# Kernel tuning notes

Measured on AMD Instinct MI355X. Metric: run time of the kernel, lower is better.

The kernel has to match this reference:

```python
import jax, jax.numpy as jnp
import numpy as np

N_CHEM = 50000
N_GENE = 50000
D = 256   # input embed size per ntype
H = 256   # hidden size
O = 256   # out size
E = 400000  # edges per etype
ETYPES = [("chemical", "ch2ge", "gene"),
          ("gene", "ge2ch", "chemical"),
          ("chemical", "ch2ch", "chemical"),
          ("gene", "ge2ge", "gene")]
N_NODES = {"chemical": N_CHEM, "gene": N_GENE}


def setup_inputs() -> dict:
    key = jax.random.key(0)
    ks = jax.random.split(key, 40)
    inp = {}
    inp["chemical_embed"] = jax.random.normal(ks[0], (N_CHEM, D), jnp.float32)
    inp["gene_embed"] = jax.random.normal(ks[1], (N_GENE, D), jnp.float32)
    i = 2
    for st, et, dt in ETYPES:
        inp[f"W1_{et}"] = jax.random.normal(ks[i], (D, H), jnp.float32) / np.float32(np.sqrt(D)); i += 1
        inp[f"b1_{et}"] = jnp.zeros((H,), jnp.float32)
        inp[f"W2_{et}"] = jax.random.normal(ks[i], (H, O), jnp.float32) / np.float32(np.sqrt(H)); i += 1
        inp[f"b2_{et}"] = jnp.zeros((O,), jnp.float32)
        inp[f"src_{et}"] = jax.random.randint(ks[i], (E,), 0, N_NODES[st], jnp.int32); i += 1
        inp[f"dst_{et}"] = jax.random.randint(ks[i], (E,), 0, N_NODES[dt], jnp.int32); i += 1
    return inp


def _rgcn_layer(h, Ws, bs, srcs, dsts):
    """One HeteroRGCNLayer: per-etype linear on src feats, copy_u + mean reduce,
    then sum across etypes per destination ntype (DGL multi_update_all 'sum')."""
    out_dim = Ws[0].shape[1]
    dt_ref = h[ETYPES[0][0]].dtype
    agg = {nt: jnp.zeros((n, out_dim), dt_ref) for nt, n in N_NODES.items()}
    for (st, et, dt), W, b, s_idx, d_idx in zip(ETYPES, Ws, bs, srcs, dsts):
        Wh = h[st] @ W + b                              # [N_src, out]
        msg = Wh[s_idx]                                 # [E, out] gather
        ssum = jax.ops.segment_sum(msg, d_idx, num_segments=N_NODES[dt])
        cnt = jax.ops.segment_sum(jnp.ones((s_idx.shape[0], 1), dt_ref), d_idx,
                                  num_segments=N_NODES[dt])
        agg[dt] = agg[dt] + ssum / jnp.maximum(cnt, 1.0)  # mean per etype
    return agg


def reference(chemical_embed, gene_embed,
              W1_ch2ge, b1_ch2ge, W1_ge2ch, b1_ge2ch, W1_ch2ch, b1_ch2ch, W1_ge2ge, b1_ge2ge,
              W2_ch2ge, b2_ch2ge, W2_ge2ch, b2_ge2ch, W2_ch2ch, b2_ch2ch, W2_ge2ge, b2_ge2ge,
              src_ch2ge, dst_ch2ge, src_ge2ch, dst_ge2ch, src_ch2ch, dst_ch2ch, src_ge2ge, dst_ge2ge):
    srcs = [src_ch2ge, src_ge2ch, src_ch2ch, src_ge2ge]
    dsts = [dst_ch2ge, dst_ge2ch, dst_ch2ch, dst_ge2ge]
    W1s = [W1_ch2ge, W1_ge2ch, W1_ch2ch, W1_ge2ge]
    b1s = [b1_ch2ge, b1_ge2ch, b1_ch2ch, b1_ge2ge]
    W2s = [W2_ch2ge, W2_ge2ch, W2_ch2ch, W2_ge2ge]
    b2s = [b2_ch2ge, b2_ge2ch, b2_ch2ch, b2_ge2ge]

    h = {"chemical": chemical_embed, "gene": gene_embed}
    h = _rgcn_layer(h, W1s, b1s, srcs, dsts)
    h = {k: jax.nn.leaky_relu(v, negative_slope=0.01) for k, v in h.items()}
    h = _rgcn_layer(h, W2s, b2s, srcs, dsts)
    return h["chemical"]
```

## Files before the change

kernel.cpp:

```cpp
#include <hip/hip_runtime.h>
#include <hip/hip_bf16.h>

#define NNODE 50000
#define DIM   256
#define EDGES 400000
#define NET   4
#define NTOT  (NET * NNODE)
#define BSH   7
#define NBUCK ((NTOT + 127) >> BSH)
#define EPB2  8192
#define CPE   49
#define NBLKT (CPE * NET)
#define NSCAN (NBUCK * NBLKT)

#define AS1 __attribute__((address_space(1)))
#define AS3 __attribute__((address_space(3)))

typedef __attribute__((ext_vector_type(8))) __bf16 bf16x8;
typedef __attribute__((ext_vector_type(4))) float f32x4;
typedef __attribute__((ext_vector_type(4))) unsigned short u16x4;
typedef __attribute__((ext_vector_type(8))) unsigned short u16x8;

__device__ __forceinline__ float bf2f(unsigned short u) {
  unsigned int x = ((unsigned int)u) << 16;
  return __builtin_bit_cast(float, x);
}
__device__ __forceinline__ unsigned short f2bf(float f) {
  __hip_bfloat16 h = __float2bfloat16(f);
  return __builtin_bit_cast(unsigned short, h);
}

__global__ void conv_f32_bf16(const float* __restrict__ in, unsigned short* __restrict__ out, int n4) {
  int i = blockIdx.x * blockDim.x + threadIdx.x;
  if (i >= n4) return;
  f32x4 v = reinterpret_cast<const f32x4*>(in)[i];
  u16x4 o;
  o[0] = f2bf(v[0]); o[1] = f2bf(v[1]); o[2] = f2bf(v[2]); o[3] = f2bf(v[3]);
  reinterpret_cast<u16x4*>(out)[i] = o;
}

__global__ void conv_wTb(const float* __restrict__ a0, const float* __restrict__ b0,
                         const float* __restrict__ a1, const float* __restrict__ b1,
                         const float* __restrict__ a2, const float* __restrict__ b2,
                         unsigned short* __restrict__ t0, unsigned short* __restrict__ t1,
                         unsigned short* __restrict__ t2) {
  int m = blockIdx.y;
  const float* A = (m == 0) ? a0 : (m == 1) ? a1 : a2;
  const float* B = (m == 0) ? b0 : (m == 1) ? b1 : b2;
  unsigned short* T = (m == 0) ? t0 : (m == 1) ? t1 : t2;
  int n = blockIdx.x, k = threadIdx.x;
  int seg = ((k >> 3) & 7) ^ (n & 7), j = k & 7;
  T[((k >> 6) * 256 + n) * 64 + seg * 8 + j]       = f2bf(A[k * 256 + n]);
  T[((4 + (k >> 6)) * 256 + n) * 64 + seg * 8 + j] = f2bf(B[k * 256 + n]);
}

__global__ void fill_f32(float* __restrict__ p, float v, int n) {
  int i = blockIdx.x * blockDim.x + threadIdx.x;
  if (i < n) p[i] = v;
}

__global__ void hist_ms(const int* __restrict__ d0, const int* __restrict__ d1,
                        const int* __restrict__ d2, const int* __restrict__ d3,
                        int* __restrict__ cnt) {
  __shared__ int h[NBUCK];
  for (int i = threadIdx.x; i < NBUCK; i += 256) h[i] = 0;
  __syncthreads();
  int t = blockIdx.y, cx = blockIdx.x;
  const int* dp = (t == 0) ? d0 : (t == 1) ? d1 : (t == 2) ? d2 : d3;
  int base = cx * EPB2;
  int lim = base + EPB2; if (lim > EDGES) lim = EDGES;
  for (int i = base + threadIdx.x; i < lim; i += 256)
    atomicAdd(&h[(t * NNODE + dp[i]) >> BSH], 1);
  __syncthreads();
  int blk = t * CPE + cx;
  for (int i = threadIdx.x; i < NBUCK; i += 256)
    cnt[i * NBLKT + blk] = h[i];
}

__global__ void scan_p1(const int* __restrict__ data, int* __restrict__ bsum, int n) {
  __shared__ int red[256];
  int base = blockIdx.x * 4096;
  int s = 0;
  #pragma unroll
  for (int j = 0; j < 16; j++) {
    int idx = base + j * 256 + threadIdx.x;
    s += (idx < n) ? data[idx] : 0;
  }
  red[threadIdx.x] = s;
  __syncthreads();
  for (int o = 128; o > 0; o >>= 1) {
    if (threadIdx.x < o) red[threadIdx.x] += red[threadIdx.x + o];
    __syncthreads();
  }
  if (threadIdx.x == 0) bsum[blockIdx.x] = red[0];
}

__global__ void scan_p2(int* __restrict__ bsum, int nb, int* __restrict__ off, int nscan,
                        int* __restrict__ S) {
  __shared__ int sh[128];
  int tid = threadIdx.x;
  int v = (tid < nb) ? bsum[tid] : 0;
  sh[tid] = v;
  __syncthreads();
  for (int o = 1; o < 128; o <<= 1) {
    int a = (tid >= o) ? sh[tid - o] : 0;
    __syncthreads();
    sh[tid] += a;
    __syncthreads();
  }
  if (tid < nb) bsum[tid] = sh[tid] - v;
  if (tid == 0) { off[nscan] = sh[127]; S[NTOT] = sh[127]; }
}

__global__ void scan_p3(int* __restrict__ data, const int* __restrict__ bsum, int n) {
  __shared__ int sh[256];
  int tid = threadIdx.x;
  int base = blockIdx.x * 4096 + tid * 16;
  int vals[16];
  int s = 0;
  #pragma unroll
  for (int j = 0; j < 16; j++) {
    vals[j] = (base + j < n) ? data[base + j] : 0;
    s += vals[j];
  }
  sh[tid] = s;
  __syncthreads();
  for (int o = 1; o < 256; o <<= 1) {
    int a = (tid >= o) ? sh[tid - o] : 0;
    __syncthreads();
    sh[tid] += a;
    __syncthreads();
  }
  int run = bsum[blockIdx.x] + sh[tid] - s;
  #pragma unroll
  for (int j = 0; j < 16; j++) {
    if (base + j < n) { data[base + j] = run; run += vals[j]; }
  }
}

__global__ void scatter_ms(const int* __restrict__ s0, const int* __restrict__ s1,
                           const int* __restrict__ s2, const int* __restrict__ s3,
                           const int* __restrict__ d0, const int* __restrict__ d1,
                           const int* __restrict__ d2, const int* __restrict__ d3,
                           const int* __restrict__ off, unsigned int* __restrict__ pairs) {
  __shared__ int cur[NBUCK];
  int t = blockIdx.y, cx = blockIdx.x;
  int blk = t * CPE + cx;
  for (int i = threadIdx.x; i < NBUCK; i += 256)
    cur[i] = off[i * NBLKT + blk];
  __syncthreads();
  const int* sp = (t == 0) ? s0 : (t == 1) ? s1 : (t == 2) ? s2 : s3;
  const int* dp = (t == 0) ? d0 : (t == 1) ? d1 : (t == 2) ? d2 : d3;
  int base = cx * EPB2;
  int lim = base + EPB2; if (lim > EDGES) lim = EDGES;
  for (int i = base + threadIdx.x; i < lim; i += 256) {
    int key = t * NNODE + dp[i];
    int slot = atomicAdd(&cur[key >> BSH], 1);
    pairs[slot] = ((unsigned int)(key & 127) << 16) | (unsigned int)sp[i];
  }
}

__global__ void bucket_final(const int* __restrict__ off, const unsigned int* __restrict__ pairs,
                             int* __restrict__ S, int* __restrict__ srcs) {
  __shared__ int lcnt[128];
  __shared__ int loff[128];
  int b = blockIdx.x;
  int tid = threadIdx.x;
  int beg = off[b * NBLKT], end = off[(b + 1) * NBLKT];
  if (tid < 128) lcnt[tid] = 0;
  __syncthreads();
  for (int e = beg + tid; e < end; e += 256)
    atomicAdd(&lcnt[pairs[e] >> 16], 1);
  __syncthreads();
  int c = (tid < 128) ? lcnt[tid] : 0;
  if (tid < 128) loff[tid] = c;
  __syncthreads();
  for (int o = 1; o < 128; o <<= 1) {
    int a = (tid < 128 && tid >= o) ? loff[tid - o] : 0;
    __syncthreads();
    if (tid < 128) loff[tid] += a;
    __syncthreads();
  }
  if (tid < 128) {
    int ex = loff[tid] - c;
    int key = (b << BSH) + tid;
    if (key < NTOT) S[key] = beg + ex;
    lcnt[tid] = ex;
  }
  __syncthreads();
  for (int e = beg + tid; e < end; e += 256) {
    unsigned int p = pairs[e];
    int lk = p >> 16;
    int slot = beg + atomicAdd(&lcnt[lk], 1);
    srcs[slot] = (int)(p & 0xFFFFu);
  }
}

#define ACC8(V)                                             \
  { _Pragma("unroll")                                       \
    for (int j = 0; j < 8; j++) acc[j] += bf2f((V)[j]); }

__device__ __forceinline__ void agg_loop(const int* __restrict__ srcs, int e0, int e1,
                                         int half, int l5,
                                         const unsigned short* __restrict__ feat, float* acc) {
  int e = e0 + half;
  u16x8 z = {};
  #define LDK(K) ((e + 2*(K) < e1)                                                    \
      ? *reinterpret_cast<const u16x8*>(feat + (size_t)srcs[e + 2*(K)] * 256 + l5 * 8) \
      : z)
  u16x8 v0 = LDK(0), v1 = LDK(1), v2 = LDK(2), v3 = LDK(3);
  while (e + 8 < e1) {
    u16x8 c0 = v0, c1 = v1, c2 = v2, c3 = v3;
    e += 8;
    v0 = LDK(0); v1 = LDK(1); v2 = LDK(2); v3 = LDK(3);
    ACC8(c0); ACC8(c1); ACC8(c2); ACC8(c3);
  }
  ACC8(v0); ACC8(v1); ACC8(v2); ACC8(v3);
  #undef LDK
}

__global__ __launch_bounds__(256) void agg_pair(
    const int* __restrict__ S, const int* __restrict__ srcs,
    const unsigned short* __restrict__ featA, int etA, unsigned short* __restrict__ outA,
    const unsigned short* __restrict__ featB, int etB, unsigned short* __restrict__ outB)
{
  int d = blockIdx.x * 4 + (threadIdx.x >> 6);
  int lane = threadIdx.x & 63;
  int half = lane >> 5, l5 = lane & 31;
  size_t obase = ((size_t)(l5 >> 3) * NNODE + d) * 64 + (((l5 & 7) ^ (d & 7)) << 3);

  int gA = etA * NNODE + d;
  int a0 = S[gA], a1 = S[gA + 1];
  int gB = etB * NNODE + d;
  int b0 = S[gB], b1 = S[gB + 1];

  {
    float acc[8] = {0,0,0,0,0,0,0,0};
    agg_loop(srcs, a0, a1, half, l5, featA, acc);
    #pragma unroll
    for (int j = 0; j < 8; j++) acc[j] += __shfl_xor(acc[j], 32);
    float dA = (float)(a1 - a0); if (dA < 1.f) dA = 1.f;
    float invA = 1.f / dA;
    if (half == 0) {
      u16x8 o;
      #pragma unroll
      for (int j = 0; j < 8; j++) o[j] = f2bf(acc[j] * invA);
      *reinterpret_cast<u16x8*>(outA + obase) = o;
    }
  }
  {
    float acc[8] = {0,0,0,0,0,0,0,0};
    agg_loop(srcs, b0, b1, half, l5, featB, acc);
    #pragma unroll
    for (int j = 0; j < 8; j++) acc[j] += __shfl_xor(acc[j], 32);
    float dB = (float)(b1 - b0); if (dB < 1.f) dB = 1.f;
    float invB = 1.f / dB;
    if (half == 1) {
      u16x8 o;
      #pragma unroll
      for (int j = 0; j < 8; j++) o[j] = f2bf(acc[j] * invB);
      *reinterpret_cast<u16x8*>(outB + obase) = o;
    }
  }
}

template<int MODE>
__global__ __launch_bounds__(256, 2) void gemm512(
    const unsigned short* __restrict__ A0, const unsigned short* __restrict__ A1,
    const unsigned short* __restrict__ WTb,
    const float* __restrict__ bA, const float* __restrict__ bB,
    const int* __restrict__ S, int etA, int etB,
    void* __restrict__ outp, int M)
{
  __shared__ char lds[2 * 40960];
  int tid = threadIdx.x;
  int m0 = blockIdx.x * 64;
  int wave = tid >> 6, lane = tid & 63;
  int wr = wave >> 1, wc = wave & 1;
  int lrow = lane & 15, kgrp = lane >> 4;

  f32x4 acc[2][8];
  #pragma unroll
  for (int a = 0; a < 2; a++)
    #pragma unroll
    for (int b = 0; b < 8; b++) acc[a][b] = (f32x4){0.f, 0.f, 0.f, 0.f};

  auto stage = [&](int ck) {
    char* buf = lds + (ck & 1) * 40960;
    const char* wsrc = (const char*)WTb + (size_t)ck * 32768 + tid * 16;
    #pragma unroll
    for (int iss = 0; iss < 8; iss++)
      __builtin_amdgcn_global_load_lds(
          (const AS1 unsigned int*)(const void*)(wsrc + iss * 4096),
          (AS3 unsigned int*)(void*)(buf + 8192 + iss * 4096 + tid * 16), 16, 0, 0);
    const char* asrc = (const char*)((ck < 4) ? A0 : A1) +
        (size_t)(ck & 3) * NNODE * 128 + (size_t)m0 * 128 + tid * 16;
    #pragma unroll
    for (int iss = 0; iss < 2; iss++)
      __builtin_amdgcn_global_load_lds(
          (const AS1 unsigned int*)(const void*)(asrc + iss * 4096),
          (AS3 unsigned int*)(void*)(buf + iss * 4096 + tid * 16), 16, 0, 0);
  };

  auto compute = [&](int ck) {
    const char* buf = lds + (ck & 1) * 40960;
    #pragma unroll
    for (int ks = 0; ks < 2; ks++) {
      int ks4 = ks << 2;
      bf16x8 a[2];
      #pragma unroll
      for (int mb = 0; mb < 2; mb++) {
        int r = 32 * wr + 16 * mb + lrow;
        a[mb] = *reinterpret_cast<const bf16x8*>(buf + r * 128 + (((ks4 | kgrp) ^ (r & 7)) << 4));
      }
      #pragma unroll
      for (int nb = 0; nb < 8; nb++) {
        int n = 128 * wc + 16 * nb + lrow;
        bf16x8 b = *reinterpret_cast<const bf16x8*>(buf + 8192 + n * 128 + (((ks4 | kgrp) ^ (n & 7)) << 4));
        acc[0][nb] = __builtin_amdgcn_mfma_f32_16x16x32_bf16(a[0], b, acc[0][nb], 0, 0, 0);
        acc[1][nb] = __builtin_amdgcn_mfma_f32_16x16x32_bf16(a[1], b, acc[1][nb], 0, 0, 0);
      }
    }
  };

  stage(0);
  for (int ck = 0; ck < 7; ck++) {
    stage(ck + 1);
    asm volatile("s_waitcnt vmcnt(10)" ::: "memory");
    asm volatile("s_barrier" ::: "memory");
    compute(ck);
    asm volatile("s_barrier" ::: "memory");
  }
  asm volatile("s_waitcnt vmcnt(0)" ::: "memory");
  asm volatile("s_barrier" ::: "memory");
  compute(7);

  #pragma unroll
  for (int mb = 0; mb < 2; mb++) {
    #pragma unroll
    for (int r = 0; r < 4; r++) {
      int row = m0 + 32 * wr + 16 * mb + kgrp * 4 + r;
      if (row >= M) continue;
      int gA = etA * NNODE + row, gB = etB * NNODE + row;
      bool hA = S[gA + 1] > S[gA];
      bool hB = S[gB + 1] > S[gB];
      #pragma unroll
      for (int nb = 0; nb < 8; nb++) {
        int col = 128 * wc + 16 * nb + lrow;
        float bias = (hA ? bA[col] : 0.f) + (hB ? bB[col] : 0.f);
        float v = acc[mb][nb][r] + bias;
        if (MODE == 0) {
          v = (v > 0.f) ? v : 0.01f * v;
          ((unsigned short*)outp)[(size_t)row * 256 + col] = f2bf(v);
        } else {
          ((float*)outp)[(size_t)row * 256 + col] = v;
        }
      }
    }
  }
}

extern "C" void kernel_launch(void* const* d_in, const int* in_sizes, int n_in,
                              void* d_out, int out_size, void* d_ws, size_t ws_size,
                              hipStream_t stream) {
  (void)in_sizes; (void)n_in;
  const float* chem = (const float*)d_in[0];
  const float* gene = (const float*)d_in[1];
  const float *W1[4], *B1[4], *W2[4], *B2[4];
  const int *SRC[4], *DST[4];
  for (int t = 0; t < 4; t++) {
    W1[t]  = (const float*)d_in[2 + 6 * t];
    B1[t]  = (const float*)d_in[3 + 6 * t];
    W2[t]  = (const float*)d_in[4 + 6 * t];
    B2[t]  = (const float*)d_in[5 + 6 * t];
    SRC[t] = (const int*)d_in[6 + 6 * t];
    DST[t] = (const int*)d_in[7 + 6 * t];
  }

  size_t off_b = 0;
  auto carve = [&](size_t bytes) -> void* {
    void* p = (char*)d_ws + off_b;
    off_b += (bytes + 255) & ~(size_t)255;
    return p;
  };
  const size_t FEAT_B = (size_t)NNODE * DIM * 2;
  unsigned short* xb_chem = (unsigned short*)carve(FEAT_B);
  unsigned short* xb_gene = (unsigned short*)carve(FEAT_B);
  unsigned short* h1_chem = (unsigned short*)carve(FEAT_B);
  unsigned short* h1_gene = (unsigned short*)carve(FEAT_B);
  unsigned short* aggA    = (unsigned short*)carve(FEAT_B);
  unsigned short* aggB    = (unsigned short*)carve(FEAT_B);
  int* S    = (int*)carve(((size_t)NTOT + 1) * 4);
  int* srcs = (int*)carve((size_t)NET * EDGES * 4);
  unsigned short* WTc1 = (unsigned short*)carve((size_t)256 * 512 * 2);
  unsigned short* WTg1 = (unsigned short*)carve((size_t)256 * 512 * 2);
  unsigned short* WTc2 = (unsigned short*)carve((size_t)256 * 512 * 2);
  unsigned int* pairs = (unsigned int*)aggA;
  int* cntoff = (int*)((char*)aggA + 6400000);
  int* bsum   = cntoff + (NSCAN + 1);

  if (off_b > ws_size) {
    fill_f32<<<(out_size + 255) / 256, 256, 0, stream>>>((float*)d_out, (float)(ws_size >> 20), out_size);
    return;
  }

  int n4 = NNODE * DIM / 4;
  conv_f32_bf16<<<(n4 + 255) / 256, 256, 0, stream>>>(chem, xb_chem, n4);
  conv_f32_bf16<<<(n4 + 255) / 256, 256, 0, stream>>>(gene, xb_gene, n4);
  conv_wTb<<<dim3(256, 3), 256, 0, stream>>>(W1[1], W1[2], W1[0], W1[3], W2[1], W2[2],
                                             WTc1, WTg1, WTc2);

  dim3 cgrid(CPE, 4);
  hist_ms<<<cgrid, 256, 0, stream>>>(DST[0], DST[1], DST[2], DST[3], cntoff);
  int nb1 = (NSCAN + 4095) / 4096;
  scan_p1<<<nb1, 256, 0, stream>>>(cntoff, bsum, NSCAN);
  scan_p2<<<1, 128, 0, stream>>>(bsum, nb1, cntoff, NSCAN, S);
  scan_p3<<<nb1, 256, 0, stream>>>(cntoff, bsum, NSCAN);
  scatter_ms<<<cgrid, 256, 0, stream>>>(SRC[0], SRC[1], SRC[2], SRC[3],
                                        DST[0], DST[1], DST[2], DST[3], cntoff, pairs);
  bucket_final<<<NBUCK, 256, 0, stream>>>(cntoff, pairs, S, srcs);

  dim3 ggrid2((NNODE + 63) / 64);
  int nagg = NNODE / 4;
  agg_pair<<<nagg, 256, 0, stream>>>(S, srcs, xb_gene, 1, aggA, xb_chem, 2, aggB);
  gemm512<0><<<ggrid2, 256, 0, stream>>>(aggA, aggB, WTc1, B1[1], B1[2], S, 1, 2, h1_chem, NNODE);
  agg_pair<<<nagg, 256, 0, stream>>>(S, srcs, xb_chem, 0, aggA, xb_gene, 3, aggB);
  gemm512<0><<<ggrid2, 256, 0, stream>>>(aggA, aggB, WTg1, B1[0], B1[3], S, 0, 3, h1_gene, NNODE);
  agg_pair<<<nagg, 256, 0, stream>>>(S, srcs, h1_gene, 1, aggA, h1_chem, 2, aggB);
  gemm512<1><<<ggrid2, 256, 0, stream>>>(aggA, aggB, WTc2, B2[1], B2[2], S, 1, 2, d_out, NNODE);
}
```

Before: 427.3 us.

## Fuse neighbor mean-aggregation into GEMM via LDS-resident aggregated tile

Replaces the separate agg_pair and gemm512 kernels with a fused kernel. Each block of 32 destination rows aggregates its neighbor features into LDS and then runs the MFMA GEMM against double-buffered weight chunks streamed in 32-wide K slices. This removes the global write and re-read of the intermediate aggregated features and three kernel launches. In exchange the M tile shrinks from 64 to 32, so the weights are re-fetched by twice as many blocks, and the weight layout is re-swizzled for the narrower K chunks. The sort scratch moves into the h1_chem buffer.

```diff
diff --git a/kernel.cpp b/kernel.cpp
--- a/kernel.cpp
+++ b/kernel.cpp
@@ -39,19 +39,20 @@
   reinterpret_cast<u16x4*>(out)[i] = o;
 }
 
-__global__ void conv_wTb(const float* __restrict__ a0, const float* __restrict__ b0,
-                         const float* __restrict__ a1, const float* __restrict__ b1,
-                         const float* __restrict__ a2, const float* __restrict__ b2,
-                         unsigned short* __restrict__ t0, unsigned short* __restrict__ t1,
-                         unsigned short* __restrict__ t2) {
+__global__ void conv_wT32(const float* __restrict__ a0, const float* __restrict__ b0,
+                          const float* __restrict__ a1, const float* __restrict__ b1,
+                          const float* __restrict__ a2, const float* __restrict__ b2,
+                          unsigned short* __restrict__ t0, unsigned short* __restrict__ t1,
+                          unsigned short* __restrict__ t2) {
   int m = blockIdx.y;
   const float* A = (m == 0) ? a0 : (m == 1) ? a1 : a2;
   const float* B = (m == 0) ? b0 : (m == 1) ? b1 : b2;
   unsigned short* T = (m == 0) ? t0 : (m == 1) ? t1 : t2;
   int n = blockIdx.x, k = threadIdx.x;
-  int seg = ((k >> 3) & 7) ^ (n & 7), j = k & 7;
-  T[((k >> 6) * 256 + n) * 64 + seg * 8 + j]       = f2bf(A[k * 256 + n]);
-  T[((4 + (k >> 6)) * 256 + n) * 64 + seg * 8 + j] = f2bf(B[k * 256 + n]);
+  int kg = (k >> 3) & 3, j = k & 7;
+  int sw = ((kg ^ (n & 3)) << 3) + j;
+  T[(k >> 5) * 8192 + n * 32 + sw]       = f2bf(A[k * 256 + n]);
+  T[(8 + (k >> 5)) * 8192 + n * 32 + sw] = f2bf(B[k * 256 + n]);
 }
 
 __global__ void fill_f32(float* __restrict__ p, float v, int n) {
@@ -219,134 +220,110 @@
   #undef LDK
 }
 
-__global__ __launch_bounds__(256) void agg_pair(
+template<int MODE>
+__global__ __launch_bounds__(256, 2) void fused_ag(
     const int* __restrict__ S, const int* __restrict__ srcs,
-    const unsigned short* __restrict__ featA, int etA, unsigned short* __restrict__ outA,
-    const unsigned short* __restrict__ featB, int etB, unsigned short* __restrict__ outB)
-{
-  int d = blockIdx.x * 4 + (threadIdx.x >> 6);
-  int lane = threadIdx.x & 63;
-  int half = lane >> 5, l5 = lane & 31;
-  size_t obase = ((size_t)(l5 >> 3) * NNODE + d) * 64 + (((l5 & 7) ^ (d & 7)) << 3);
-
-  int gA = etA * NNODE + d;
-  int a0 = S[gA], a1 = S[gA + 1];
-  int gB = etB * NNODE + d;
-  int b0 = S[gB], b1 = S[gB + 1];
-
-  {
-    float acc[8] = {0,0,0,0,0,0,0,0};
-    agg_loop(srcs, a0, a1, half, l5, featA, acc);
-    #pragma unroll
-    for (int j = 0; j < 8; j++) acc[j] += __shfl_xor(acc[j], 32);
-    float dA = (float)(a1 - a0); if (dA < 1.f) dA = 1.f;
-    float invA = 1.f / dA;
-    if (half == 0) {
-      u16x8 o;
-      #pragma unroll
-      for (int j = 0; j < 8; j++) o[j] = f2bf(acc[j] * invA);
-      *reinterpret_cast<u16x8*>(outA + obase) = o;
-    }
-  }
-  {
-    float acc[8] = {0,0,0,0,0,0,0,0};
-    agg_loop(srcs, b0, b1, half, l5, featB, acc);
-    #pragma unroll
-    for (int j = 0; j < 8; j++) acc[j] += __shfl_xor(acc[j], 32);
-    float dB = (float)(b1 - b0); if (dB < 1.f) dB = 1.f;
-    float invB = 1.f / dB;
-    if (half == 1) {
-      u16x8 o;
-      #pragma unroll
-      for (int j = 0; j < 8; j++) o[j] = f2bf(acc[j] * invB);
-      *reinterpret_cast<u16x8*>(outB + obase) = o;
-    }
-  }
-}
-
-template<int MODE>
-__global__ __launch_bounds__(256, 2) void gemm512(
-    const unsigned short* __restrict__ A0, const unsigned short* __restrict__ A1,
+    const unsigned short* __restrict__ featA, int etA,
+    const unsigned short* __restrict__ featB, int etB,
     const unsigned short* __restrict__ WTb,
     const float* __restrict__ bA, const float* __restrict__ bB,
-    const int* __restrict__ S, int etA, int etB,
     void* __restrict__ outp, int M)
 {
-  __shared__ char lds[2 * 40960];
+  __shared__ char lds[32768 + 2 * 16384];
   int tid = threadIdx.x;
-  int m0 = blockIdx.x * 64;
   int wave = tid >> 6, lane = tid & 63;
-  int wr = wave >> 1, wc = wave & 1;
+  int half = lane >> 5, l5 = lane & 31;
   int lrow = lane & 15, kgrp = lane >> 4;
-
-  f32x4 acc[2][8];
+  int m0 = blockIdx.x * 32;
+
+  auto stageB = [&](int ck) {
+    char* buf = lds + 32768 + (ck & 1) * 16384;
+    const char* src = (const char*)WTb + (size_t)ck * 16384 + tid * 16;
+    #pragma unroll
+    for (int iss = 0; iss < 4; iss++)
+      __builtin_amdgcn_global_load_lds(
+          (const AS1 unsigned int*)(const void*)(src + iss * 4096),
+          (AS3 unsigned int*)(void*)(buf + iss * 4096 + tid * 16), 16, 0, 0);
+  };
+  stageB(0);
+
+  for (int i = 0; i < 8; i++) {
+    int r = wave * 8 + i;
+    int d = m0 + r;
+    int a0 = 0, a1 = 0, b0 = 0, b1 = 0;
+    if (d < M) {
+      int gA = etA * NNODE + d;
+      a0 = S[gA]; a1 = S[gA + 1];
+      int gB = etB * NNODE + d;
+      b0 = S[gB]; b1 = S[gB + 1];
+    }
+    float accA[8] = {0,0,0,0,0,0,0,0}, accB[8] = {0,0,0,0,0,0,0,0};
+    { float* acc = accA; agg_loop(srcs, a0, a1, half, l5, featA, acc); }
+    { float* acc = accB; agg_loop(srcs, b0, b1, half, l5, featB, acc); }
+    #pragma unroll
+    for (int j = 0; j < 8; j++) {
+      accA[j] += __shfl_xor(accA[j], 32);
+      accB[j] += __shfl_xor(accB[j], 32);
+    }
+    float dA = (float)(a1 - a0); if (dA < 1.f) dA = 1.f;
+    float dB = (float)(b1 - b0); if (dB < 1.f) dB = 1.f;
+    float invA = 1.f / dA, invB = 1.f / dB;
+    u16x8 o;
+    int s;
+    if (half == 0) {
+      #pragma unroll
+      for (int j = 0; j < 8; j++) o[j] = f2bf(accA[j] * invA);
+      s = l5;
+    } else {
+      #pragma unroll
+      for (int j = 0; j < 8; j++) o[j] = f2bf(accB[j] * invB);
+      s = 32 + l5;
+    }
+    *reinterpret_cast<u16x8*>(lds + r * 1024 + ((s ^ (r & 7)) << 4)) = o;
+  }
+
+  f32x4 acc[2][4];
   #pragma unroll
   for (int a = 0; a < 2; a++)
     #pragma unroll
-    for (int b = 0; b < 8; b++) acc[a][b] = (f32x4){0.f, 0.f, 0.f, 0.f};
-
-  auto stage = [&](int ck) {
-    char* buf = lds + (ck & 1) * 40960;
-    const char* wsrc = (const char*)WTb + (size_t)ck * 32768 + tid * 16;
-    #pragma unroll
-    for (int iss = 0; iss < 8; iss++)
-      __builtin_amdgcn_global_load_lds(
-          (const AS1 unsigned int*)(const void*)(wsrc + iss * 4096),
-          (AS3 unsigned int*)(void*)(buf + 8192 + iss * 4096 + tid * 16), 16, 0, 0);
-    const char* asrc = (const char*)((ck < 4) ? A0 : A1) +
-        (size_t)(ck & 3) * NNODE * 128 + (size_t)m0 * 128 + tid * 16;
-    #pragma unroll
-    for (int iss = 0; iss < 2; iss++)
-      __builtin_amdgcn_global_load_lds(
-          (const AS1 unsigned int*)(const void*)(asrc + iss * 4096),
-          (AS3 unsigned int*)(void*)(buf + iss * 4096 + tid * 16), 16, 0, 0);
+    for (int b = 0; b < 4; b++) acc[a][b] = (f32x4){0.f, 0.f, 0.f, 0.f};
+
+  auto compute = [&](int ck) {
+    const char* bbuf = lds + 32768 + (ck & 1) * 16384;
+    int kseg = ck * 4 + kgrp;
+    bf16x8 a[2];
+    #pragma unroll
+    for (int mb = 0; mb < 2; mb++) {
+      int r = mb * 16 + lrow;
+      a[mb] = *reinterpret_cast<const bf16x8*>(lds + r * 1024 + ((kseg ^ (r & 7)) << 4));
+    }
+    #pragma unroll
+    for (int nb = 0; nb < 4; nb++) {
+      int n = wave * 64 + nb * 16 + lrow;
+      bf16x8 b = *reinterpret_cast<const bf16x8*>(bbuf + n * 64 + ((kgrp ^ (n & 3)) << 4));
+      acc[0][nb] = __builtin_amdgcn_mfma_f32_16x16x32_bf16(a[0], b, acc[0][nb], 0, 0, 0);
+      acc[1][nb] = __builtin_amdgcn_mfma_f32_16x16x32_bf16(a[1], b, acc[1][nb], 0, 0, 0);
+    }
   };
 
-  auto compute = [&](int ck) {
-    const char* buf = lds + (ck & 1) * 40960;
-    #pragma unroll
-    for (int ks = 0; ks < 2; ks++) {
-      int ks4 = ks << 2;
-      bf16x8 a[2];
-      #pragma unroll
-      for (int mb = 0; mb < 2; mb++) {
-        int r = 32 * wr + 16 * mb + lrow;
-        a[mb] = *reinterpret_cast<const bf16x8*>(buf + r * 128 + (((ks4 | kgrp) ^ (r & 7)) << 4));
-      }
-      #pragma unroll
-      for (int nb = 0; nb < 8; nb++) {
-        int n = 128 * wc + 16 * nb + lrow;
-        bf16x8 b = *reinterpret_cast<const bf16x8*>(buf + 8192 + n * 128 + (((ks4 | kgrp) ^ (n & 7)) << 4));
-        acc[0][nb] = __builtin_amdgcn_mfma_f32_16x16x32_bf16(a[0], b, acc[0][nb], 0, 0, 0);
-        acc[1][nb] = __builtin_amdgcn_mfma_f32_16x16x32_bf16(a[1], b, acc[1][nb], 0, 0, 0);
-      }
-    }
-  };
-
-  stage(0);
-  for (int ck = 0; ck < 7; ck++) {
-    stage(ck + 1);
-    asm volatile("s_waitcnt vmcnt(10)" ::: "memory");
-    asm volatile("s_barrier" ::: "memory");
+  for (int ck = 0; ck < 16; ck++) {
+    __syncthreads();
+    if (ck < 15) stageB(ck + 1);
     compute(ck);
-    asm volatile("s_barrier" ::: "memory");
-  }
-  asm volatile("s_waitcnt vmcnt(0)" ::: "memory");
-  asm volatile("s_barrier" ::: "memory");
-  compute(7);
+  }
 
   #pragma unroll
   for (int mb = 0; mb < 2; mb++) {
     #pragma unroll
     for (int r = 0; r < 4; r++) {
-      int row = m0 + 32 * wr + 16 * mb + kgrp * 4 + r;
+      int row = m0 + mb * 16 + kgrp * 4 + r;
       if (row >= M) continue;
       int gA = etA * NNODE + row, gB = etB * NNODE + row;
       bool hA = S[gA + 1] > S[gA];
       bool hB = S[gB + 1] > S[gB];
       #pragma unroll
-      for (int nb = 0; nb < 8; nb++) {
-        int col = 128 * wc + 16 * nb + lrow;
+      for (int nb = 0; nb < 4; nb++) {
+        int col = wave * 64 + 16 * nb + lrow;
         float bias = (hA ? bA[col] : 0.f) + (hB ? bB[col] : 0.f);
         float v = acc[mb][nb][r] + bias;
         if (MODE == 0) {
@@ -388,15 +365,13 @@
   unsigned short* xb_gene = (unsigned short*)carve(FEAT_B);
   unsigned short* h1_chem = (unsigned short*)carve(FEAT_B);
   unsigned short* h1_gene = (unsigned short*)carve(FEAT_B);
-  unsigned short* aggA    = (unsigned short*)carve(FEAT_B);
-  unsigned short* aggB    = (unsigned short*)carve(FEAT_B);
   int* S    = (int*)carve(((size_t)NTOT + 1) * 4);
   int* srcs = (int*)carve((size_t)NET * EDGES * 4);
   unsigned short* WTc1 = (unsigned short*)carve((size_t)256 * 512 * 2);
   unsigned short* WTg1 = (unsigned short*)carve((size_t)256 * 512 * 2);
   unsigned short* WTc2 = (unsigned short*)carve((size_t)256 * 512 * 2);
-  unsigned int* pairs = (unsigned int*)aggA;
-  int* cntoff = (int*)((char*)aggA + 6400000);
+  unsigned int* pairs = (unsigned int*)h1_chem;
+  int* cntoff = (int*)((char*)h1_chem + 6400000);
   int* bsum   = cntoff + (NSCAN + 1);
 
   if (off_b > ws_size) {
@@ -407,8 +382,8 @@
   int n4 = NNODE * DIM / 4;
   conv_f32_bf16<<<(n4 + 255) / 256, 256, 0, stream>>>(chem, xb_chem, n4);
   conv_f32_bf16<<<(n4 + 255) / 256, 256, 0, stream>>>(gene, xb_gene, n4);
-  conv_wTb<<<dim3(256, 3), 256, 0, stream>>>(W1[1], W1[2], W1[0], W1[3], W2[1], W2[2],
-                                             WTc1, WTg1, WTc2);
+  conv_wT32<<<dim3(256, 3), 256, 0, stream>>>(W1[1], W1[2], W1[0], W1[3], W2[1], W2[2],
+                                              WTc1, WTg1, WTc2);
 
   dim3 cgrid(CPE, 4);
   hist_ms<<<cgrid, 256, 0, stream>>>(DST[0], DST[1], DST[2], DST[3], cntoff);
@@ -420,12 +395,11 @@
                                         DST[0], DST[1], DST[2], DST[3], cntoff, pairs);
   bucket_final<<<NBUCK, 256, 0, stream>>>(cntoff, pairs, S, srcs);
 
-  dim3 ggrid2((NNODE + 63) / 64);
-  int nagg = NNODE / 4;
-  agg_pair<<<nagg, 256, 0, stream>>>(S, srcs, xb_gene, 1, aggA, xb_chem, 2, aggB);
-  gemm512<0><<<ggrid2, 256, 0, stream>>>(aggA, aggB, WTc1, B1[1], B1[2], S, 1, 2, h1_chem, NNODE);
-  agg_pair<<<nagg, 256, 0, stream>>>(S, srcs, xb_chem, 0, aggA, xb_gene, 3, aggB);
-  gemm512<0><<<ggrid2, 256, 0, stream>>>(aggA, aggB, WTg1, B1[0], B1[3], S, 0, 3, h1_gene, NNODE);
-  agg_pair<<<nagg, 256, 0, stream>>>(S, srcs, h1_gene, 1, aggA, h1_chem, 2, aggB);
-  gemm512<1><<<ggrid2, 256, 0, stream>>>(aggA, aggB, WTc2, B2[1], B2[2], S, 1, 2, d_out, NNODE);
-}
+  int nfb = (NNODE + 31) / 32;
+  fused_ag<0><<<nfb, 256, 0, stream>>>(S, srcs, xb_gene, 1, xb_chem, 2,
+                                       WTc1, B1[1], B1[2], h1_chem, NNODE);
+  fused_ag<0><<<nfb, 256, 0, stream>>>(S, srcs, xb_chem, 0, xb_gene, 3,
+                                       WTg1, B1[0], B1[3], h1_gene, NNODE);
+  fused_ag<1><<<nfb, 256, 0, stream>>>(S, srcs, h1_gene, 1, h1_chem, 2,
+                                       WTc2, B2[1], B2[2], d_out, NNODE);
+}
```

Result: slower. 656.9 us (+53.7%).
